# Performance work log

Hardware: AMD Instinct MI355X
Metric: run time of the kernel (lower is better)

## Reference

```python
import jax, jax.numpy as jnp
import numpy as np

NUM_CLASSES = 1000
NUM_NODES = 1111  # 1000 leaves + 100 + 10 + 1 root
BATCH = 32768


def _build_hierarchy():
    """Deterministic 10-ary 3-level hierarchy standing in for heirachy_graph.p.

    Returns:
      A: [NUM_NODES, NUM_CLASSES] float32, A[n, l] = 1 if node n lies on leaf l's
         path to root (including leaf l itself). probs = outputs @ A.T reproduces
         the per-sample dict accumulation probs[node] += val.
      W: [NUM_CLASSES, NUM_NODES] float32 path-weight vectors:
         W[t, path[j]] += 2^-(j+1) for path root->t, plus the extra
         W[t, t] += 2^-len(path) term from the source.
    """
    parent = {}
    for l in range(1000):
        parent[l] = 1000 + l // 10
    for k in range(100):
        parent[1000 + k] = 1100 + k // 10
    for m in range(10):
        parent[1100 + m] = 1110
    parent[1110] = None

    A = np.zeros((NUM_NODES, NUM_CLASSES), dtype=np.float32)
    for l in range(NUM_CLASSES):
        node = l
        A[node, l] = 1.0
        while parent[node] is not None:
            node = parent[node]
            A[node, l] += 1.0

    W = np.zeros((NUM_CLASSES, NUM_NODES), dtype=np.float32)
    for t in range(NUM_CLASSES):
        path = [t]
        node = t
        while parent[node] is not None:
            node = parent[node]
            path = [node] + path
        for j, p in enumerate(path):
            W[t, p] += 2.0 ** (-(j + 1))
        W[t, t] += 2.0 ** (-len(path))  # extra target term in the source
    return A, W


def setup_inputs() -> dict:
    key = jax.random.key(0)
    k1, k2 = jax.random.split(key)
    outputs = jax.random.normal(k1, (BATCH, NUM_CLASSES), dtype=jnp.float32)
    target = jax.random.randint(k2, (BATCH,), 0, NUM_CLASSES, dtype=jnp.int64)
    A_np, W_np = _build_hierarchy()
    return {
        "outputs": outputs,
        "target": target,
        "A": jnp.asarray(A_np),
        "W": jnp.asarray(W_np),
    }


def reference(outputs, target, A, W):
    # probs[b, n] = sum over leaves l under node n of outputs[b, l]
    probs = outputs @ A.T                      # [B, NUM_NODES]
    w = W[target]                               # [B, NUM_NODES] gather per target
    win = jnp.einsum("bn,bn->b", probs, w)     # [B]
    return jnp.sum(1.0 - win)                  # scalar loss
```

## Files before the change

kernel.cpp:

```cpp
#include <hip/hip_runtime.h>


constexpr int BATCH   = 32768;
constexpr int NCLS    = 1000;
constexpr int N4      = BATCH * NCLS / 4;
constexpr int BLOCKS  = 2048;
constexpr int THREADS = 256;
constexpr int ROWS_PER_BLOCK = BATCH / BLOCKS;
constexpr int STRIDE  = BLOCKS * THREADS;

__global__ __launch_bounds__(THREADS) void hloss_part(
    const float* __restrict__ outputs,
    const int*   __restrict__ target,
    float* __restrict__ partials)
{
    __shared__ float red[4];
    const int lane = threadIdx.x & 63;
    const int wid  = threadIdx.x >> 6;
    float win = 0.0f;

    {
        const int rowbase = blockIdx.x * ROWS_PER_BLOCK + wid * 4;
        const int h  = lane >> 5;
        const int ln = lane & 31;
        int tmine = 0;
        if (lane < 4) tmine = target[rowbase + lane];
        #pragma unroll
        for (int pass = 0; pass < 2; ++pass) {
            const int r = pass * 2 + h;
            const int t = __shfl(tmine, r, 64);
            const int b = rowbase + r;
            const int lo100 = (t / 100) * 100;
            const int lo10  = (t / 10)  * 10;
            if (ln < 25) {
                const int l0 = lo100 + ln * 4;
                const float4 v = *reinterpret_cast<const float4*>(
                    outputs + (size_t)b * NCLS + l0);
                const float xs[4] = {v.x, v.y, v.z, v.w};
                #pragma unroll
                for (int j = 0; j < 4; ++j) {
                    const int l = l0 + j;
                    float w = 0.25f;
                    if ((unsigned)(l - lo10) < 10u) w += 0.125f;
                    if (l == t)                     w += 0.125f;
                    win = fmaf(xs[j], w, win);
                }
            }
        }
    }

    {
        const float4* src = reinterpret_cast<const float4*>(outputs);
        const int tid    = blockIdx.x * THREADS + threadIdx.x;
        const int stride = STRIDE;
        float a0 = 0.f, a1 = 0.f, a2 = 0.f, a3 = 0.f;
        int i = tid;
        for (; i + 3 * stride < N4; i += 4 * stride) {
            const float4 v0 = src[i];
            const float4 v1 = src[i + stride];
            const float4 v2 = src[i + 2 * stride];
            const float4 v3 = src[i + 3 * stride];
            a0 += v0.x + v0.y + v0.z + v0.w;
            a1 += v1.x + v1.y + v1.z + v1.w;
            a2 += v2.x + v2.y + v2.z + v2.w;
            a3 += v3.x + v3.y + v3.z + v3.w;
        }
        for (; i < N4; i += stride) {
            const float4 v = src[i];
            a0 += v.x + v.y + v.z + v.w;
        }
        win = fmaf(0.5f, (a0 + a1) + (a2 + a3), win);
    }

    #pragma unroll
    for (int off = 32; off > 0; off >>= 1)
        win += __shfl_xor(win, off, 64);
    if (lane == 0) red[wid] = win;
    __syncthreads();
    if (threadIdx.x == 0)
        partials[blockIdx.x] = red[0] + red[1] + red[2] + red[3];
}

__global__ __launch_bounds__(THREADS) void hloss_final(
    const float* __restrict__ partials,
    float* __restrict__ out)
{
    __shared__ float red[4];
    const int lane = threadIdx.x & 63;
    const int wid  = threadIdx.x >> 6;
    float s = 0.0f;
    for (int i = threadIdx.x; i < BLOCKS; i += THREADS)
        s += partials[i];
    #pragma unroll
    for (int off = 32; off > 0; off >>= 1)
        s += __shfl_xor(s, off, 64);
    if (lane == 0) red[wid] = s;
    __syncthreads();
    if (threadIdx.x == 0)
        out[0] = (float)BATCH - ((red[0] + red[1]) + (red[2] + red[3]));
}

extern "C" void kernel_launch(void* const* d_in, const int* in_sizes, int n_in,
                              void* d_out, int out_size, void* d_ws, size_t ws_size,
                              hipStream_t stream) {
    const float* outputs = (const float*)d_in[0];
    const int*   target  = (const int*)d_in[1];
    float* out      = (float*)d_out;
    float* partials = (float*)d_ws;

    hloss_part <<<dim3(BLOCKS), dim3(THREADS), 0, stream>>>(outputs, target, partials);
    hloss_final<<<dim3(1),      dim3(THREADS), 0, stream>>>(partials, out);
}
```

Before: 31.86 us.

## Fuse targeted-window and full-row sums into single per-row weighted pass

```diff
diff --git a/kernel.cpp b/kernel.cpp
--- a/kernel.cpp
+++ b/kernel.cpp
@@ -3,11 +3,25 @@
 
 constexpr int BATCH   = 32768;
 constexpr int NCLS    = 1000;
-constexpr int N4      = BATCH * NCLS / 4;
+constexpr int NQ      = NCLS / 4;
 constexpr int BLOCKS  = 2048;
 constexpr int THREADS = 256;
-constexpr int ROWS_PER_BLOCK = BATCH / BLOCKS;
-constexpr int STRIDE  = BLOCKS * THREADS;
+
+__device__ __forceinline__ float wdot4(const float4 v, int l0,
+                                       int t, int lo100, int lo10) {
+    const float xs[4] = {v.x, v.y, v.z, v.w};
+    float acc = 0.0f;
+    #pragma unroll
+    for (int j = 0; j < 4; ++j) {
+        const int l = l0 + j;
+        float w = 0.5f;
+        if ((unsigned)(l - lo100) < 100u) w += 0.25f;
+        if ((unsigned)(l - lo10)  < 10u)  w += 0.125f;
+        if (l == t)                       w += 0.125f;
+        acc = fmaf(xs[j], w, acc);
+    }
+    return acc;
+}
 
 __global__ __launch_bounds__(THREADS) void hloss_part(
     const float* __restrict__ outputs,
@@ -17,60 +31,34 @@
     __shared__ float red[4];
     const int lane = threadIdx.x & 63;
     const int wid  = threadIdx.x >> 6;
-    float win = 0.0f;
+    const int rowbase = blockIdx.x * 16 + wid * 4;
 
-    {
-        const int rowbase = blockIdx.x * ROWS_PER_BLOCK + wid * 4;
-        const int h  = lane >> 5;
-        const int ln = lane & 31;
-        int tmine = 0;
-        if (lane < 4) tmine = target[rowbase + lane];
-        #pragma unroll
-        for (int pass = 0; pass < 2; ++pass) {
-            const int r = pass * 2 + h;
-            const int t = __shfl(tmine, r, 64);
-            const int b = rowbase + r;
-            const int lo100 = (t / 100) * 100;
-            const int lo10  = (t / 10)  * 10;
-            if (ln < 25) {
-                const int l0 = lo100 + ln * 4;
-                const float4 v = *reinterpret_cast<const float4*>(
-                    outputs + (size_t)b * NCLS + l0);
-                const float xs[4] = {v.x, v.y, v.z, v.w};
-                #pragma unroll
-                for (int j = 0; j < 4; ++j) {
-                    const int l = l0 + j;
-                    float w = 0.25f;
-                    if ((unsigned)(l - lo10) < 10u) w += 0.125f;
-                    if (l == t)                     w += 0.125f;
-                    win = fmaf(xs[j], w, win);
-                }
-            }
-        }
+    int tmine = 0;
+    if (lane < 4) tmine = target[rowbase + lane];
+    const int t0 = __shfl(tmine, 0, 64);
+    const int t1 = __shfl(tmine, 1, 64);
+    const int t2 = __shfl(tmine, 2, 64);
+    const int t3 = __shfl(tmine, 3, 64);
+    const int a0 = (t0 / 100) * 100, b0 = (t0 / 10) * 10;
+    const int a1 = (t1 / 100) * 100, b1 = (t1 / 10) * 10;
+    const int a2 = (t2 / 100) * 100, b2 = (t2 / 10) * 10;
+    const int a3 = (t3 / 100) * 100, b3 = (t3 / 10) * 10;
+
+    const float* base = outputs + (size_t)rowbase * NCLS;
+    float w0 = 0.f, w1 = 0.f, w2 = 0.f, w3 = 0.f;
+
+    for (int c4 = lane; c4 < NQ; c4 += 64) {
+        const float4 v0 = *reinterpret_cast<const float4*>(base + 0 * NCLS + c4 * 4);
+        const float4 v1 = *reinterpret_cast<const float4*>(base + 1 * NCLS + c4 * 4);
+        const float4 v2 = *reinterpret_cast<const float4*>(base + 2 * NCLS + c4 * 4);
+        const float4 v3 = *reinterpret_cast<const float4*>(base + 3 * NCLS + c4 * 4);
+        const int l0 = c4 * 4;
+        w0 += wdot4(v0, l0, t0, a0, b0);
+        w1 += wdot4(v1, l0, t1, a1, b1);
+        w2 += wdot4(v2, l0, t2, a2, b2);
+        w3 += wdot4(v3, l0, t3, a3, b3);
     }
-
-    {
-        const float4* src = reinterpret_cast<const float4*>(outputs);
-        const int tid    = blockIdx.x * THREADS + threadIdx.x;
-        const int stride = STRIDE;
-        float a0 = 0.f, a1 = 0.f, a2 = 0.f, a3 = 0.f;
-        int i = tid;
-        for (; i + 3 * stride < N4; i += 4 * stride) {
-            const float4 v0 = src[i];
-            const float4 v1 = src[i + stride];
-            const float4 v2 = src[i + 2 * stride];
-            const float4 v3 = src[i + 3 * stride];
-            a0 += v0.x + v0.y + v0.z + v0.w;
-            a1 += v1.x + v1.y + v1.z + v1.w;
-            a2 += v2.x + v2.y + v2.z + v2.w;
-            a3 += v3.x + v3.y + v3.z + v3.w;
-        }
-        for (; i < N4; i += stride) {
-            const float4 v = src[i];
-            a0 += v.x + v.y + v.z + v.w;
-        }
-        win = fmaf(0.5f, (a0 + a1) + (a2 + a3), win);
-    }
+    float win = (w0 + w1) + (w2 + w3);
 
     #pragma unroll
     for (int off = 32; off > 0; off >>= 1)
@@ -78,7 +66,7 @@
     if (lane == 0) red[wid] = win;
     __syncthreads();
     if (threadIdx.x == 0)
-        partials[blockIdx.x] = red[0] + red[1] + red[2] + red[3];
+        partials[blockIdx.x] = (red[0] + red[1]) + (red[2] + red[3]);
 }
 
 __global__ __launch_bounds__(THREADS) void hloss_final(
```

New measurement: 29.48 us. 1.08x faster.
